# Kernel tuning notes

Measured on AMD Instinct MI355X. Metric: run time of the kernel, lower is better.

## Reference

```python
import jax, jax.numpy as jnp
import numpy as np

DECAY = 0.1
EPS = 1e-5


def setup_inputs() -> dict:
    key = jax.random.key(0)
    k1, k2, k3, k4 = jax.random.split(key, 4)
    N, K, D = 262144, 1024, 64
    x = jax.random.normal(k1, (N, D), dtype=jnp.float32)
    embed = jax.random.normal(k2, (K, D), dtype=jnp.float32) * 0.01
    cluster_size = jax.random.uniform(k3, (K,), dtype=jnp.float32)
    embed_avg = jax.random.normal(k4, (K, D), dtype=jnp.float32) * 0.01
    return {"x": x, "embed": embed, "cluster_size": cluster_size, "embed_avg": embed_avg}


def reference(x, embed, cluster_size, embed_avg):
    # x: [N, D] flattened latents; embed: [K, D] codebook
    N, D = x.shape
    K = embed.shape[0]

    # Squared Euclidean distance (same argmin as torch.cdist p=2).
    x2 = jnp.sum(x * x, axis=-1, keepdims=True)            # [N, 1]
    e2 = jnp.sum(embed * embed, axis=-1)                   # [K]
    dist = x2 - 2.0 * jnp.einsum('nd,kd->nk', x, embed) + e2[None, :]  # [N, K]
    embed_ind = jnp.argmin(dist, axis=-1)                  # [N] int

    # Quantize: gather nearest codes.
    quantize = embed[embed_ind]                            # [N, D]

    # --- EMA codebook update (no-grad in the original) ---
    xs = jax.lax.stop_gradient(x)
    bins = jax.ops.segment_sum(jnp.ones((N,), dtype=x.dtype), embed_ind,
                               num_segments=K)             # [K] bincount
    embed_sum = jax.ops.segment_sum(xs, embed_ind, num_segments=K)  # [K, D] scatter-add

    cluster_size_new = cluster_size * DECAY + bins * (1.0 - DECAY)
    embed_avg_new = embed_avg * DECAY + embed_sum * (1.0 - DECAY)

    # Laplace smoothing then normalize to get the updated codebook.
    n = jnp.sum(cluster_size_new)
    cs_smoothed = (cluster_size_new + EPS) / (n + K * EPS) * n
    embed_normalized = embed_avg_new / cs_smoothed[:, None]  # [K, D]

    return quantize, embed_ind, cluster_size_new, embed_avg_new, embed_normalized
```

## Files before the change

kernel.cpp:

```cpp
#include <hip/hip_runtime.h>
#include <hip/hip_bf16.h>


#define NROWS 262144
#define KCODES 1024
#define DDIM 64
#define CAPL 8

typedef __attribute__((ext_vector_type(8)))  short short8;
typedef __attribute__((ext_vector_type(16))) float f32x16;

__device__ __forceinline__ unsigned short f2bf(float f) {
    unsigned u = __float_as_uint(f);
    unsigned r = u + 0x7fffu + ((u >> 16) & 1u);
    return (unsigned short)(r >> 16);
}

__global__ __launch_bounds__(256) void vq_prep(
    const float* __restrict__ embed, unsigned short* __restrict__ eb,
    float* __restrict__ e2f, float* __restrict__ enmax2)
{
    const int k = blockIdx.x * 256 + threadIdx.x;
    const float* er = embed + (size_t)k * DDIM;
    float s = 0.f;
    #pragma unroll
    for (int d = 0; d < DDIM; ++d) { float v = er[d]; s = fmaf(v, v, s); }
    e2f[k] = s;
    #pragma unroll
    for (int d = 0; d < DDIM; ++d) eb[(size_t)k * DDIM + d] = f2bf(er[d]);
    atomicMax((int*)enmax2, __float_as_int(s));
}

__global__ __launch_bounds__(1024, 4) void vq_phaseA(
    const float* __restrict__ x, const unsigned short* __restrict__ eb,
    const float* __restrict__ e2f, const float* __restrict__ enmax2,
    float* __restrict__ out_ind, int* __restrict__ candg, int* __restrict__ cntg,
    int* __restrict__ wl, int* __restrict__ gcount,
    int* __restrict__ wl2, int* __restrict__ gcount2, int* __restrict__ bins_i)
{
    __shared__ __align__(16) unsigned short ebs[65536];
    __shared__ float norm2L[512];
    __shared__ int   cntL[512];
    __shared__ int   candL[512][CAPL];
    __shared__ int   mcount, mbase, mcount2, mbase2;

    const int t    = threadIdx.x;
    const int lane = t & 63;
    const int wid  = t >> 6;
    const int lo   = lane & 31;
    const int hi   = lane >> 5;
    const int rowb = blockIdx.x * 512;
    const int myrow = rowb + wid * 32 + lo;

    short8 af[4];
    float xsq = 0.f;
    {
        const float* xr = x + (size_t)myrow * DDIM;
        #pragma unroll
        for (int i = 0; i < 4; ++i) {
            const float4 a = *reinterpret_cast<const float4*>(xr + 16 * i + 8 * hi);
            const float4 b = *reinterpret_cast<const float4*>(xr + 16 * i + 8 * hi + 4);
            short8 f;
            f[0] = (short)f2bf(a.x); f[1] = (short)f2bf(a.y);
            f[2] = (short)f2bf(a.z); f[3] = (short)f2bf(a.w);
            f[4] = (short)f2bf(b.x); f[5] = (short)f2bf(b.y);
            f[6] = (short)f2bf(b.z); f[7] = (short)f2bf(b.w);
            af[i] = f;
            xsq = fmaf(a.x, a.x, xsq); xsq = fmaf(a.y, a.y, xsq);
            xsq = fmaf(a.z, a.z, xsq); xsq = fmaf(a.w, a.w, xsq);
            xsq = fmaf(b.x, b.x, xsq); xsq = fmaf(b.y, b.y, xsq);
            xsq = fmaf(b.z, b.z, xsq); xsq = fmaf(b.w, b.w, xsq);
        }
    }
    const float n2full = xsq + __shfl_xor(xsq, 32);
    if (hi == 0) norm2L[wid * 32 + lo] = n2full;

    #pragma unroll
    for (int it = 0; it < 8; ++it) {
        const int f16  = t + it * 1024;
        const int ch   = f16 >> 8;
        const int r    = f16 & 255;
        const int code = r >> 3, slot = r & 7;
        const short8 v = *reinterpret_cast<const short8*>(eb + (size_t)f16 * 8);
        *reinterpret_cast<short8*>((char*)ebs + ch * 4096 + code * 128 +
                                   ((slot ^ (code & 7)) << 4)) = v;
    }
    if (t < 512) cntL[t] = 0;
    if (t == 0) { mcount = 0; mcount2 = 0; }
    const float en2 = *enmax2;
    __syncthreads();

    f32x16 best;
    #pragma unroll
    for (int r = 0; r < 16; ++r) best[r] = 3.4e38f;

    for (int ch = 0; ch < 32; ++ch) {
        short8 bfr[4];
        #pragma unroll
        for (int i = 0; i < 4; ++i) {
            const int slot = 2 * i + hi;
            bfr[i] = *reinterpret_cast<const short8*>(
                (char*)ebs + ch * 4096 + lo * 128 + (((slot ^ (lo & 7))) << 4));
        }
        const float e2l = e2f[ch * 32 + lo];
        f32x16 acc;
        #pragma unroll
        for (int r = 0; r < 16; ++r) acc[r] = 0.f;
        #pragma unroll
        for (int i = 0; i < 4; ++i)
            acc = __builtin_amdgcn_mfma_f32_32x32x16_bf16(af[i], bfr[i], acc, 0, 0, 0);
        #pragma unroll
        for (int r = 0; r < 16; ++r)
            best[r] = fminf(best[r], fmaf(-2.f, acc[r], e2l));
    }

    #pragma unroll
    for (int r = 0; r < 16; ++r) {
        float v = best[r];
        v = fminf(v, __shfl_xor(v, 1));  v = fminf(v, __shfl_xor(v, 2));
        v = fminf(v, __shfl_xor(v, 4));  v = fminf(v, __shfl_xor(v, 8));
        v = fminf(v, __shfl_xor(v, 16));
        const int rr = (r & 3) + 8 * (r >> 2) + 4 * hi;
        const float nr2 = norm2L[wid * 32 + rr];
        best[r] = v + 0.015625f * sqrtf(nr2 * en2) + 1e-4f;
    }

    for (int ch = 0; ch < 32; ++ch) {
        short8 bfr[4];
        #pragma unroll
        for (int i = 0; i < 4; ++i) {
            const int slot = 2 * i + hi;
            bfr[i] = *reinterpret_cast<const short8*>(
                (char*)ebs + ch * 4096 + lo * 128 + (((slot ^ (lo & 7))) << 4));
        }
        const float e2l = e2f[ch * 32 + lo];
        f32x16 acc;
        #pragma unroll
        for (int r = 0; r < 16; ++r) acc[r] = 0.f;
        #pragma unroll
        for (int i = 0; i < 4; ++i)
            acc = __builtin_amdgcn_mfma_f32_32x32x16_bf16(af[i], bfr[i], acc, 0, 0, 0);
        #pragma unroll
        for (int r = 0; r < 16; ++r) {
            const float d0 = fmaf(-2.f, acc[r], e2l);
            if (d0 <= best[r]) {
                const int rr = (r & 3) + 8 * (r >> 2) + 4 * hi;
                const int rl = wid * 32 + rr;
                const int idx = atomicAdd(&cntL[rl], 1);
                if (idx < CAPL) candL[rl][idx] = ch * 32 + lo;
            }
        }
    }
    __syncthreads();

    int my = -1, my2 = -1, c = 0;
    if (t < 512) {
        c = cntL[t];
        if (c == 1) {
            const int code = candL[t][0];
            out_ind[rowb + t] = (float)code;
            atomicAdd(bins_i + code, 1);
        }
        else if (c <= CAPL)   my  = atomicAdd(&mcount, 1);
        else                  my2 = atomicAdd(&mcount2, 1);
    }
    __syncthreads();
    if (t == 0) { mbase = atomicAdd(gcount, mcount); mbase2 = atomicAdd(gcount2, mcount2); }
    __syncthreads();
    if (my >= 0) {
        const int row = rowb + t;
        wl[mbase + my] = row;
        cntg[row] = c;
        #pragma unroll
        for (int j = 0; j < CAPL; ++j)
            if (j < c) candg[row * 8 + j] = candL[t][j];
    }
    if (my2 >= 0) wl2[mbase2 + my2] = rowb + t;
}

__global__ __launch_bounds__(256) void vq_rerank1(
    const float* __restrict__ x, const float* __restrict__ embed,
    const float* __restrict__ e2f, const int* __restrict__ wl,
    const int* __restrict__ gcount, const int* __restrict__ cntg,
    const int* __restrict__ candg, float* __restrict__ out_ind,
    int* __restrict__ bins_i)
{
    const int n = *gcount;
    for (int i = blockIdx.x * 256 + threadIdx.x; i < n; i += gridDim.x * 256) {
        const int row = wl[i];
        float xv[DDIM];
        {
            const float4* xp = reinterpret_cast<const float4*>(x + (size_t)row * DDIM);
            float4 xq[16];
            #pragma unroll
            for (int q = 0; q < 16; ++q) xq[q] = xp[q];
            #pragma unroll
            for (int q = 0; q < 16; ++q) {
                xv[q*4+0] = xq[q].x; xv[q*4+1] = xq[q].y;
                xv[q*4+2] = xq[q].z; xv[q*4+3] = xq[q].w;
            }
        }
        float x2 = 0.f;
        #pragma unroll
        for (int d = 0; d < DDIM; ++d) x2 = fmaf(xv[d], xv[d], x2);

        const int c = cntg[row];
        float bv = 3.4e38f; int bk = 0x7fffffff;
        for (int ci = 0; ci < c; ++ci) {
            const int k = candg[row * 8 + ci];
            const float4* ep = reinterpret_cast<const float4*>(embed + (size_t)k * DDIM);
            float dot = 0.f;
            #pragma unroll
            for (int q = 0; q < 16; ++q) {
                const float4 e4 = ep[q];
                dot = fmaf(xv[q*4+0], e4.x, dot);
                dot = fmaf(xv[q*4+1], e4.y, dot);
                dot = fmaf(xv[q*4+2], e4.z, dot);
                dot = fmaf(xv[q*4+3], e4.w, dot);
            }
            const float dist = (x2 - 2.0f * dot) + e2f[k];
            if (dist < bv || (dist == bv && k < bk)) { bv = dist; bk = k; }
        }
        out_ind[row] = (float)bk;
        atomicAdd(bins_i + bk, 1);
    }
}

__global__ __launch_bounds__(256) void vq_rerank2(
    const float* __restrict__ x, const float* __restrict__ embed,
    const float* __restrict__ e2f, const int* __restrict__ wl2,
    const int* __restrict__ gcount2, float* __restrict__ out_ind,
    int* __restrict__ bins_i)
{
    const int t    = threadIdx.x;
    const int lane = t & 63;
    const int gw   = (blockIdx.x * 256 + t) >> 6;
    const int nw   = (gridDim.x * 256) >> 6;
    const int n    = *gcount2;

    for (int e = gw; e < n; e += nw) {
        const int row = wl2[e];
        float xv[DDIM];
        {
            const float4* xp = reinterpret_cast<const float4*>(x + (size_t)row * DDIM);
            #pragma unroll
            for (int q = 0; q < 16; ++q) {
                const float4 v = xp[q];
                xv[q*4+0] = v.x; xv[q*4+1] = v.y; xv[q*4+2] = v.z; xv[q*4+3] = v.w;
            }
        }
        float x2 = 0.f;
        #pragma unroll
        for (int d = 0; d < DDIM; ++d) x2 = fmaf(xv[d], xv[d], x2);

        float bv = 3.4e38f; int bk = 0x7fffffff;
        for (int k = lane; k < KCODES; k += 64) {
            const float* er = embed + (size_t)k * DDIM;
            float dot = 0.f;
            #pragma unroll
            for (int d = 0; d < DDIM; ++d) dot = fmaf(xv[d], er[d], dot);
            const float dist = (x2 - 2.0f * dot) + e2f[k];
            if (dist < bv) { bv = dist; bk = k; }
        }
        #pragma unroll
        for (int s = 1; s < 64; s <<= 1) {
            const float ov = __shfl_xor(bv, s);
            const int   ok = __shfl_xor(bk, s);
            if (ov < bv || (ov == bv && ok < bk)) { bv = ov; bk = ok; }
        }
        if (lane == 0) { out_ind[row] = (float)bk; atomicAdd(bins_i + bk, 1); }
    }
}

__global__ __launch_bounds__(1024) void vq_prefix(
    const int* __restrict__ bins_i, int* __restrict__ offs, int* __restrict__ cursor)
{
    __shared__ int s[KCODES];
    const int t = threadIdx.x;
    const int b = bins_i[t];
    s[t] = b;
    __syncthreads();
    for (int d = 1; d < KCODES; d <<= 1) {
        const int v = (t >= d) ? s[t - d] : 0;
        __syncthreads();
        s[t] += v;
        __syncthreads();
    }
    const int excl = s[t] - b;
    offs[t] = excl;
    cursor[t] = excl;
}

__global__ __launch_bounds__(256) void vq_scatter(
    const float* __restrict__ out_ind, int* __restrict__ cursor, int* __restrict__ sorted)
{
    const int row  = blockIdx.x * 256 + threadIdx.x;
    const int code = (int)out_ind[row];
    const int pos  = atomicAdd(cursor + code, 1);
    sorted[pos] = (code << 20) | row;
}

__global__ __launch_bounds__(256) void vq_reduce(
    const float* __restrict__ x, const int* __restrict__ sorted,
    float* __restrict__ esum)
{
    const int t = threadIdx.x, lane = t & 63, w = t >> 6;
    const int p0 = (blockIdx.x * 4 + w) * 64;

    int cur = sorted[p0] >> 20;
    float acc = 0.f;
    #pragma unroll 4
    for (int i = 0; i < 64; i += 4) {
        const int4 e4 = *reinterpret_cast<const int4*>(sorted + p0 + i);
        const float v0 = x[(size_t)(e4.x & 0xFFFFF) * DDIM + lane];
        const float v1 = x[(size_t)(e4.y & 0xFFFFF) * DDIM + lane];
        const float v2 = x[(size_t)(e4.z & 0xFFFFF) * DDIM + lane];
        const float v3 = x[(size_t)(e4.w & 0xFFFFF) * DDIM + lane];
        const int c0 = e4.x >> 20, c1 = e4.y >> 20, c2 = e4.z >> 20, c3 = e4.w >> 20;
        if (c0 != cur) { unsafeAtomicAdd(esum + cur * DDIM + lane, acc); acc = 0.f; cur = c0; }
        acc += v0;
        if (c1 != cur) { unsafeAtomicAdd(esum + cur * DDIM + lane, acc); acc = 0.f; cur = c1; }
        acc += v1;
        if (c2 != cur) { unsafeAtomicAdd(esum + cur * DDIM + lane, acc); acc = 0.f; cur = c2; }
        acc += v2;
        if (c3 != cur) { unsafeAtomicAdd(esum + cur * DDIM + lane, acc); acc = 0.f; cur = c3; }
        acc += v3;
    }
    unsafeAtomicAdd(esum + cur * DDIM + lane, acc);
}

__global__ __launch_bounds__(1024) void vq_finalize(
    const float* __restrict__ cluster_size, const float* __restrict__ embed_avg,
    const int* __restrict__ bins_i, float* __restrict__ out_cs,
    float* __restrict__ out_eavg, float* __restrict__ out_enorm)
{
    __shared__ float red[KCODES];
    __shared__ float css[KCODES];
    const int t = threadIdx.x;

    const float csn = cluster_size[t] * 0.1f + (float)bins_i[t] * 0.9f;
    red[t] = csn;
    __syncthreads();
    for (int s = 512; s > 0; s >>= 1) {
        if (t < s) red[t] += red[t + s];
        __syncthreads();
    }
    const float n = red[0];
    out_cs[t] = csn;
    css[t] = (csn + 1e-5f) / (n + (float)(KCODES * 1e-5)) * n;
    __syncthreads();

    #pragma unroll
    for (int i = 0; i < 16; ++i) {
        const int f4 = t + i * 1024;
        const int k  = f4 >> 4;
        const float4 ea = reinterpret_cast<const float4*>(embed_avg)[f4];
        const float4 su = reinterpret_cast<const float4*>(out_eavg)[f4];
        const float  cc = css[k];
        float4 ean, en;
        ean.x = ea.x * 0.1f + su.x * 0.9f; en.x = ean.x / cc;
        ean.y = ea.y * 0.1f + su.y * 0.9f; en.y = ean.y / cc;
        ean.z = ea.z * 0.1f + su.z * 0.9f; en.z = ean.z / cc;
        ean.w = ea.w * 0.1f + su.w * 0.9f; en.w = ean.w / cc;
        reinterpret_cast<float4*>(out_eavg)[f4]  = ean;
        reinterpret_cast<float4*>(out_enorm)[f4] = en;
    }
}

__global__ __launch_bounds__(256) void vq_quant(
    const float* __restrict__ out_ind, const float* __restrict__ embed,
    float* __restrict__ out_q)
{
    __shared__ int inds[256];
    const int t = threadIdx.x;
    const int row0 = blockIdx.x * 256;
    inds[t] = (int)out_ind[row0 + t];
    __syncthreads();
    #pragma unroll
    for (int i = 0; i < 16; ++i) {
        const int f = t + i * 256;
        const int r = f >> 4, dq = f & 15;
        const int code = inds[r];
        const float4 ev = *reinterpret_cast<const float4*>(
            embed + (size_t)code * DDIM + dq * 4);
        *reinterpret_cast<float4*>(out_q + (size_t)(row0 + r) * DDIM + dq * 4) = ev;
    }
}

extern "C" void kernel_launch(void* const* d_in, const int* in_sizes, int n_in,
                              void* d_out, int out_size, void* d_ws, size_t ws_size,
                              hipStream_t stream)
{
    const float* x            = (const float*)d_in[0];
    const float* embed        = (const float*)d_in[1];
    const float* cluster_size = (const float*)d_in[2];
    const float* embed_avg    = (const float*)d_in[3];

    float* out      = (float*)d_out;
    float* out_q    = out;
    float* out_ind  = out_q + (size_t)NROWS * DDIM;
    float* out_cs   = out_ind + NROWS;
    float* out_eavg = out_cs + KCODES;
    float* out_en   = out_eavg + (size_t)KCODES * DDIM;

    unsigned short* eb = (unsigned short*)out_en;
    float* e2f = out_en + 32768;

    int* S      = (int*)out_q;
    int* candg  = S;
    int* cntg   = S + 2097152;
    int* wl     = S + 2359296;
    int* wl2    = S + 2621440;
    int* sorted = S + 2883584;
    int* bins_i = S + 3145728;
    int* gcount = bins_i + KCODES;
    int* gcount2= gcount + 1;
    float* enmax2 = (float*)(gcount2 + 1);
    int* offs   = gcount2 + 2;
    int* cursor = offs + KCODES;

    hipMemsetAsync(bins_i, 0, (KCODES + 3) * sizeof(int), stream);
    hipMemsetAsync(out_eavg, 0, (size_t)KCODES * DDIM * sizeof(float), stream);

    vq_prep    <<<KCODES / 256, 256, 0, stream>>>(embed, eb, e2f, enmax2);
    vq_phaseA  <<<NROWS / 512, 1024, 0, stream>>>(x, eb, e2f, enmax2, out_ind,
                                                  candg, cntg, wl, gcount,
                                                  wl2, gcount2, bins_i);
    vq_rerank1 <<<512, 256, 0, stream>>>(x, embed, e2f, wl, gcount, cntg, candg,
                                         out_ind, bins_i);
    vq_rerank2 <<<128, 256, 0, stream>>>(x, embed, e2f, wl2, gcount2, out_ind, bins_i);
    vq_prefix  <<<1, 1024, 0, stream>>>(bins_i, offs, cursor);
    vq_scatter <<<NROWS / 256, 256, 0, stream>>>(out_ind, cursor, sorted);
    vq_reduce  <<<NROWS / 256, 256, 0, stream>>>(x, sorted, out_eavg);
    vq_finalize<<<1, 1024, 0, stream>>>(cluster_size, embed_avg, bins_i,
                                        out_cs, out_eavg, out_en);
    vq_quant   <<<NROWS / 256, 256, 0, stream>>>(out_ind, embed, out_q);
}
```

Before: 307.5 us.

## Halve phaseA block and stage codebook in two LDS halves

The phaseA kernel now uses 512-thread blocks covering 256 rows and keeps only half the bf16 codebook (64 KB) in shared memory at a time. It stages and sweeps each half in turn for both passes, visiting the halves in the order 0,1,1,0 so the resident half is reused across the pass boundary. The per-code squared norms are preloaded into registers instead of being read from global memory inside the loops. This reduces LDS per block so more blocks can be resident, at the cost of extra codebook restaging, more barriers, and twice as many blocks each reloading the codebook.

New measurement: 310.5 us. About the same (+1.0%).

```diff
diff --git a/kernel.cpp b/kernel.cpp
--- a/kernel.cpp
+++ b/kernel.cpp
@@ -31,17 +31,81 @@
     atomicMax((int*)enmax2, __float_as_int(s));
 }
 
-__global__ __launch_bounds__(1024, 4) void vq_phaseA(
+#define STAGE(H)                                                              \
+    _Pragma("unroll")                                                         \
+    for (int it = 0; it < 8; ++it) {                                          \
+        const int f16  = t + it * 512;                                        \
+        const int ch   = f16 >> 8;                                            \
+        const int r    = f16 & 255;                                           \
+        const int code = r >> 3, slot = r & 7;                                \
+        const short8 v = *reinterpret_cast<const short8*>(                    \
+            eb + (size_t)(H) * 32768 + (size_t)f16 * 8);                      \
+        *reinterpret_cast<short8*>((char*)ebs + ch * 4096 + code * 128 +      \
+                                   ((slot ^ (code & 7)) << 4)) = v;           \
+    }
+
+#define SWEEP1(E2ARR)                                                         \
+    _Pragma("unroll")                                                         \
+    for (int ch = 0; ch < 16; ++ch) {                                         \
+        short8 bfr[4];                                                        \
+        _Pragma("unroll")                                                     \
+        for (int i = 0; i < 4; ++i) {                                         \
+            const int slot = 2 * i + hi;                                      \
+            bfr[i] = *reinterpret_cast<const short8*>(                        \
+                (char*)ebs + ch * 4096 + lo * 128 + ((slot ^ (lo & 7)) << 4));\
+        }                                                                     \
+        const float e2l = E2ARR[ch];                                          \
+        f32x16 acc;                                                           \
+        _Pragma("unroll")                                                     \
+        for (int r = 0; r < 16; ++r) acc[r] = 0.f;                            \
+        _Pragma("unroll")                                                     \
+        for (int i = 0; i < 4; ++i)                                           \
+            acc = __builtin_amdgcn_mfma_f32_32x32x16_bf16(af[i], bfr[i], acc, 0, 0, 0); \
+        _Pragma("unroll")                                                     \
+        for (int r = 0; r < 16; ++r)                                          \
+            best[r] = fminf(best[r], fmaf(-2.f, acc[r], e2l));                \
+    }
+
+#define SWEEP2(E2ARR, CBASE)                                                  \
+    _Pragma("unroll")                                                         \
+    for (int ch = 0; ch < 16; ++ch) {                                         \
+        short8 bfr[4];                                                        \
+        _Pragma("unroll")                                                     \
+        for (int i = 0; i < 4; ++i) {                                         \
+            const int slot = 2 * i + hi;                                      \
+            bfr[i] = *reinterpret_cast<const short8*>(                        \
+                (char*)ebs + ch * 4096 + lo * 128 + ((slot ^ (lo & 7)) << 4));\
+        }                                                                     \
+        const float e2l = E2ARR[ch];                                          \
+        f32x16 acc;                                                           \
+        _Pragma("unroll")                                                     \
+        for (int r = 0; r < 16; ++r) acc[r] = 0.f;                            \
+        _Pragma("unroll")                                                     \
+        for (int i = 0; i < 4; ++i)                                           \
+            acc = __builtin_amdgcn_mfma_f32_32x32x16_bf16(af[i], bfr[i], acc, 0, 0, 0); \
+        _Pragma("unroll")                                                     \
+        for (int r = 0; r < 16; ++r) {                                        \
+            const float d0 = fmaf(-2.f, acc[r], e2l);                         \
+            if (d0 <= best[r]) {                                              \
+                const int rr = (r & 3) + 8 * (r >> 2) + 4 * hi;               \
+                const int rl = wid * 32 + rr;                                 \
+                const int idx = atomicAdd(&cntL[rl], 1);                      \
+                if (idx < CAPL) candL[rl][idx] = (CBASE) + ch * 32 + lo;      \
+            }                                                                 \
+        }                                                                     \
+    }
+
+__global__ __launch_bounds__(512, 4) void vq_phaseA(
     const float* __restrict__ x, const unsigned short* __restrict__ eb,
     const float* __restrict__ e2f, const float* __restrict__ enmax2,
     float* __restrict__ out_ind, int* __restrict__ candg, int* __restrict__ cntg,
     int* __restrict__ wl, int* __restrict__ gcount,
     int* __restrict__ wl2, int* __restrict__ gcount2, int* __restrict__ bins_i)
 {
-    __shared__ __align__(16) unsigned short ebs[65536];
-    __shared__ float norm2L[512];
-    __shared__ int   cntL[512];
-    __shared__ int   candL[512][CAPL];
+    __shared__ __align__(16) unsigned short ebs[32768];
+    __shared__ float norm2L[256];
+    __shared__ int   cntL[256];
+    __shared__ int   candL[256][CAPL];
     __shared__ int   mcount, mbase, mcount2, mbase2;
 
     const int t    = threadIdx.x;
@@ -49,7 +113,7 @@
     const int wid  = t >> 6;
     const int lo   = lane & 31;
     const int hi   = lane >> 5;
-    const int rowb = blockIdx.x * 512;
+    const int rowb = blockIdx.x * 256;
     const int myrow = rowb + wid * 32 + lo;
 
     short8 af[4];
@@ -75,44 +139,27 @@
     const float n2full = xsq + __shfl_xor(xsq, 32);
     if (hi == 0) norm2L[wid * 32 + lo] = n2full;
 
-    #pragma unroll
-    for (int it = 0; it < 8; ++it) {
-        const int f16  = t + it * 1024;
-        const int ch   = f16 >> 8;
-        const int r    = f16 & 255;
-        const int code = r >> 3, slot = r & 7;
-        const short8 v = *reinterpret_cast<const short8*>(eb + (size_t)f16 * 8);
-        *reinterpret_cast<short8*>((char*)ebs + ch * 4096 + code * 128 +
-                                   ((slot ^ (code & 7)) << 4)) = v;
-    }
-    if (t < 512) cntL[t] = 0;
+    float e2h0[16], e2h1[16];
+    #pragma unroll
+    for (int c = 0; c < 16; ++c) e2h0[c] = e2f[c * 32 + lo];
+    #pragma unroll
+    for (int c = 0; c < 16; ++c) e2h1[c] = e2f[(16 + c) * 32 + lo];
+
+    if (t < 256) cntL[t] = 0;
     if (t == 0) { mcount = 0; mcount2 = 0; }
     const float en2 = *enmax2;
-    __syncthreads();
 
     f32x16 best;
     #pragma unroll
     for (int r = 0; r < 16; ++r) best[r] = 3.4e38f;
 
-    for (int ch = 0; ch < 32; ++ch) {
-        short8 bfr[4];
-        #pragma unroll
-        for (int i = 0; i < 4; ++i) {
-            const int slot = 2 * i + hi;
-            bfr[i] = *reinterpret_cast<const short8*>(
-                (char*)ebs + ch * 4096 + lo * 128 + (((slot ^ (lo & 7))) << 4));
-        }
-        const float e2l = e2f[ch * 32 + lo];
-        f32x16 acc;
-        #pragma unroll
-        for (int r = 0; r < 16; ++r) acc[r] = 0.f;
-        #pragma unroll
-        for (int i = 0; i < 4; ++i)
-            acc = __builtin_amdgcn_mfma_f32_32x32x16_bf16(af[i], bfr[i], acc, 0, 0, 0);
-        #pragma unroll
-        for (int r = 0; r < 16; ++r)
-            best[r] = fminf(best[r], fmaf(-2.f, acc[r], e2l));
-    }
+    STAGE(0)
+    __syncthreads();
+    SWEEP1(e2h0)
+    __syncthreads();
+    STAGE(1)
+    __syncthreads();
+    SWEEP1(e2h1)
 
     #pragma unroll
     for (int r = 0; r < 16; ++r) {
@@ -125,36 +172,15 @@
         best[r] = v + 0.015625f * sqrtf(nr2 * en2) + 1e-4f;
     }
 
-    for (int ch = 0; ch < 32; ++ch) {
-        short8 bfr[4];
-        #pragma unroll
-        for (int i = 0; i < 4; ++i) {
-            const int slot = 2 * i + hi;
-            bfr[i] = *reinterpret_cast<const short8*>(
-                (char*)ebs + ch * 4096 + lo * 128 + (((slot ^ (lo & 7))) << 4));
-        }
-        const float e2l = e2f[ch * 32 + lo];
-        f32x16 acc;
-        #pragma unroll
-        for (int r = 0; r < 16; ++r) acc[r] = 0.f;
-        #pragma unroll
-        for (int i = 0; i < 4; ++i)
-            acc = __builtin_amdgcn_mfma_f32_32x32x16_bf16(af[i], bfr[i], acc, 0, 0, 0);
-        #pragma unroll
-        for (int r = 0; r < 16; ++r) {
-            const float d0 = fmaf(-2.f, acc[r], e2l);
-            if (d0 <= best[r]) {
-                const int rr = (r & 3) + 8 * (r >> 2) + 4 * hi;
-                const int rl = wid * 32 + rr;
-                const int idx = atomicAdd(&cntL[rl], 1);
-                if (idx < CAPL) candL[rl][idx] = ch * 32 + lo;
-            }
-        }
-    }
+    SWEEP2(e2h1, 512)
+    __syncthreads();
+    STAGE(0)
+    __syncthreads();
+    SWEEP2(e2h0, 0)
     __syncthreads();
 
     int my = -1, my2 = -1, c = 0;
-    if (t < 512) {
+    if (t < 256) {
         c = cntL[t];
         if (c == 1) {
             const int code = candL[t][0];
@@ -423,9 +449,9 @@
     hipMemsetAsync(out_eavg, 0, (size_t)KCODES * DDIM * sizeof(float), stream);
 
     vq_prep    <<<KCODES / 256, 256, 0, stream>>>(embed, eb, e2f, enmax2);
-    vq_phaseA  <<<NROWS / 512, 1024, 0, stream>>>(x, eb, e2f, enmax2, out_ind,
-                                                  candg, cntg, wl, gcount,
-                                                  wl2, gcount2, bins_i);
+    vq_phaseA  <<<NROWS / 256, 512, 0, stream>>>(x, eb, e2f, enmax2, out_ind,
+                                                 candg, cntg, wl, gcount,
+                                                 wl2, gcount2, bins_i);
     vq_rerank1 <<<512, 256, 0, stream>>>(x, embed, e2f, wl, gcount, cntg, candg,
                                          out_ind, bins_i);
     vq_rerank2 <<<128, 256, 0, stream>>>(x, embed, e2f, wl2, gcount2, out_ind, bins_i);
```
